# Performance work log

Hardware: AMD Instinct MI355X
Metric: run time of the kernel (lower is better)

## Reference

```python
import jax, jax.numpy as jnp
import numpy as np

N, E = 100000, 600000
IN, H = 164, 128
NH = 4  # attention heads over embed_dim H//4 = 32


def layer_norm(x, g, b, eps=1e-5):
    m = x.mean(-1, keepdims=True)
    v = x.var(-1, keepdims=True)
    return (x - m) * jax.lax.rsqrt(v + eps) * g + b


def gcn_conv(x, W, b, src, dst, n):
    # PyG GCNConv: add self-loops, symmetric D^{-1/2}(A+I)D^{-1/2} normalization.
    deg = jnp.ones((n,), x.dtype).at[dst].add(1.0)  # degree of A+I on target nodes
    dinv = jax.lax.rsqrt(deg)
    xw = x @ W  # [n, out]
    msg = xw[src] * (dinv[src] * dinv[dst])[:, None]  # gather + edge-norm
    agg = jax.ops.segment_sum(msg, dst, num_segments=n)  # scatter-add
    agg = agg + xw * (dinv * dinv)[:, None]  # self-loop term
    return agg + b


def mha_seq1(x, Wq, bq, Wk, bk, Wv, bv, Wo, bo):
    # nn.MultiheadAttention with seq_len==1: softmax over a single key -> weights==1.
    dh = x.shape[-1] // NH
    q = (x @ Wq + bq).reshape(-1, NH, dh)
    k = (x @ Wk + bk).reshape(-1, NH, dh)
    v = (x @ Wv + bv).reshape(-1, NH, dh)
    scores = jnp.sum(q * k, -1, keepdims=True) / jnp.sqrt(jnp.float32(dh))  # [n,NH,1]
    attn = jax.nn.softmax(scores[..., None], axis=-1)[..., 0]  # all ones, kept for fidelity
    out = (attn * v).reshape(-1, NH * dh)
    return out @ Wo + bo


def setup_inputs() -> dict:
    key = jax.random.key(0)
    ks = jax.random.split(key, 16)

    def kaiming(k, i, o):
        return jax.random.normal(k, (i, o), jnp.float32) * (2.0 / i) ** 0.5

    Ha, Hb, Hc = H, H // 2, H // 4  # 128, 64, 32
    return {
        "x": jax.random.normal(ks[0], (N, IN), jnp.float32),
        "edge_index": jax.random.randint(ks[1], (2, E), 0, N),
        "Wi": kaiming(ks[2], IN, Ha), "bi": jnp.zeros((Ha,), jnp.float32),
        "g1": jnp.ones((Ha,), jnp.float32), "b1": jnp.zeros((Ha,), jnp.float32),
        "Wg1": kaiming(ks[3], Ha, Ha), "bg1": jnp.zeros((Ha,), jnp.float32),
        "Wg2": kaiming(ks[4], Ha, Hb), "bg2": jnp.zeros((Hb,), jnp.float32),
        "g2": jnp.ones((Hb,), jnp.float32), "b2": jnp.zeros((Hb,), jnp.float32),
        "Wg3": kaiming(ks[5], Hb, Hc), "bg3": jnp.zeros((Hc,), jnp.float32),
        "Wq": kaiming(ks[6], Hc, Hc), "bq": jnp.zeros((Hc,), jnp.float32),
        "Wk": kaiming(ks[7], Hc, Hc), "bk": jnp.zeros((Hc,), jnp.float32),
        "Wv": kaiming(ks[8], Hc, Hc), "bv": jnp.zeros((Hc,), jnp.float32),
        "Wo": kaiming(ks[9], Hc, Hc), "bo": jnp.zeros((Hc,), jnp.float32),
        "Wc1": kaiming(ks[10], Hc, H // 8), "bc1": jnp.zeros((H // 8,), jnp.float32),
        "Wc2": kaiming(ks[11], H // 8, 32), "bc2": jnp.zeros((32,), jnp.float32),
        "Wc3": kaiming(ks[12], 32, 1), "bc3": jnp.zeros((1,), jnp.float32),
    }


def reference(x, edge_index, Wi, bi, g1, b1, Wg1, bg1, Wg2, bg2, g2, b2,
              Wg3, bg3, Wq, bq, Wk, bk, Wv, bv, Wo, bo,
              Wc1, bc1, Wc2, bc2, Wc3, bc3):
    src, dst = edge_index[0], edge_index[1]
    n = x.shape[0]
    # dropout layers are identity in eval mode
    h = layer_norm(jax.nn.relu(x @ Wi + bi), g1, b1)
    h1 = jax.nn.relu(gcn_conv(h, Wg1, bg1, src, dst, n)) + h
    h2 = layer_norm(jax.nn.relu(gcn_conv(h1, Wg2, bg2, src, dst, n)), g2, b2)
    h3 = jax.nn.relu(gcn_conv(h2, Wg3, bg3, src, dst, n))
    h3 = mha_seq1(h3, Wq, bq, Wk, bk, Wv, bv, Wo, bo)
    h3 = jax.nn.relu(h3 @ Wc1 + bc1)
    h3 = jax.nn.relu(h3 @ Wc2 + bc2)
    return (h3 @ Wc3 + bc3)[:, 0]
```

## Files before the change

kernel.cpp:

```cpp
#include <hip/hip_runtime.h>


typedef __attribute__((ext_vector_type(8))) _Float16 f16x8;
typedef __attribute__((ext_vector_type(4))) _Float16 f16x4;
typedef __attribute__((ext_vector_type(4))) float f32x4;

__global__ void k_count(const int* __restrict__ dst, int* __restrict__ counts, int e) {
  int i = blockIdx.x * blockDim.x + threadIdx.x;
  if (i < e) atomicAdd(&counts[dst[i]], 1);
}

__global__ __launch_bounds__(256) void k_scan_part(
    const int* __restrict__ counts, int* __restrict__ bsums, int n) {
  int tid = threadIdx.x;
  int i0 = blockIdx.x * 1024 + tid * 4;
  int s = 0;
#pragma unroll
  for (int k = 0; k < 4; k++) { int i = i0 + k; if (i < n) s += counts[i]; }
#pragma unroll
  for (int d = 1; d < 64; d <<= 1) s += __shfl_xor(s, d);
  __shared__ int wsum[4];
  int lane = tid & 63, w = tid >> 6;
  if (lane == 0) wsum[w] = s;
  __syncthreads();
  if (tid == 0) bsums[blockIdx.x] = wsum[0] + wsum[1] + wsum[2] + wsum[3];
}

__global__ __launch_bounds__(128) void k_scan_top(int* __restrict__ bsums, int nb) {
  int tid = threadIdx.x;
  int orig = (tid < nb) ? bsums[tid] : 0;
  int v = orig;
  int lane = tid & 63, w = tid >> 6;
#pragma unroll
  for (int d = 1; d < 64; d <<= 1) { int t = __shfl_up(v, d); if (lane >= d) v += t; }
  __shared__ int ws[2];
  if (lane == 63) ws[w] = v;
  __syncthreads();
  if (w == 1) v += ws[0];
  if (tid < nb) bsums[tid] = v - orig;
}

__global__ __launch_bounds__(256) void k_scan_down(
    int* __restrict__ counts, const int* __restrict__ bsums,
    int* __restrict__ offsets, float* __restrict__ dinv, int n, int e) {
  int tid = threadIdx.x;
  int i0 = blockIdx.x * 1024 + tid * 4;
  int c[4]; int tsum = 0;
#pragma unroll
  for (int k = 0; k < 4; k++) { int i = i0 + k; c[k] = (i < n) ? counts[i] : 0; tsum += c[k]; }
  int v = tsum;
  int lane = tid & 63, w = tid >> 6;
#pragma unroll
  for (int d = 1; d < 64; d <<= 1) { int t = __shfl_up(v, d); if (lane >= d) v += t; }
  __shared__ int wsum[4];
  if (lane == 63) wsum[w] = v;
  __syncthreads();
  int wadd = 0;
#pragma unroll
  for (int q = 0; q < 4; q++) if (q < w) wadd += wsum[q];
  int run = (v - tsum) + wadd + bsums[blockIdx.x];
#pragma unroll
  for (int k = 0; k < 4; k++) {
    int i = i0 + k;
    if (i < n) {
      offsets[i] = run;
      dinv[i] = rsqrtf((float)(c[k] + 1));
      counts[i] = 0;
    }
    run += c[k];
  }
  if (blockIdx.x == 0 && tid == 0) offsets[n] = e;
}

__global__ void k_fill(const int* __restrict__ src, const int* __restrict__ dst,
                       const int* __restrict__ offsets, int* __restrict__ cursor,
                       const float* __restrict__ dinv, int2* __restrict__ csr, int e) {
  int i = blockIdx.x * blockDim.x + threadIdx.x;
  if (i >= e) return;
  int s = src[i], d = dst[i];
  int pos = atomicAdd(&cursor[d], 1);
  csr[offsets[d] + pos] = make_int2(s, __float_as_int(dinv[s] * dinv[d]));
}

__device__ __forceinline__ void pack_hi(const float* __restrict__ W,
                                        _Float16* __restrict__ dst,
                                        int K, int N, int u) {
  int lane = u & 63; int rest = u >> 6; int CT = N >> 4;
  int ct = rest % CT, ks = rest / CT;
  int gcol = ct * 16 + (lane & 15);
  int gk0 = ks * 32 + (lane >> 4) * 8;
  size_t o = (size_t)(ks * CT + ct) * 512 + lane * 8;
#pragma unroll
  for (int i = 0; i < 8; i++) {
    float v = (gk0 + i < K) ? W[(size_t)(gk0 + i) * N + gcol] : 0.0f;
    dst[o + i] = (_Float16)v;
  }
}

__device__ __forceinline__ void pack_hl(const float* __restrict__ W,
                                        _Float16* __restrict__ dst,
                                        int K, int N, int u) {
  int lane = u & 63; int rest = u >> 6; int CT = N >> 4;
  int ct = rest % CT, ks = rest / CT;
  int gcol = ct * 16 + (lane & 15);
  int gk0 = ks * 32 + (lane >> 4) * 8;
  size_t oh = (size_t)((ks * CT + ct) * 2) * 512 + lane * 8;
#pragma unroll
  for (int i = 0; i < 8; i++) {
    float v = (gk0 + i < K) ? W[(size_t)(gk0 + i) * N + gcol] : 0.0f;
    _Float16 h = (_Float16)v;
    dst[oh + i] = h;
    dst[oh + 512 + i] = (_Float16)(v - (float)h);
  }
}

__global__ void k_setup(const float* __restrict__ Wi, const float* __restrict__ Wg1,
                        const float* __restrict__ Wg2, const float* __restrict__ Wg3,
                        _Float16* __restrict__ pWi, _Float16* __restrict__ pWg1,
                        _Float16* __restrict__ pWg2, _Float16* __restrict__ pWg3,
                        int* __restrict__ counts, int n) {
  int b = blockIdx.x;
  if (b < 25) {
    int t = b * 256 + threadIdx.x;
    if (t < 3072) pack_hi(Wi, pWi, 164, 128, t);
    else if (t < 5120) pack_hl(Wg1, pWg1, 128, 128, t - 3072);
    else if (t < 6144) pack_hl(Wg2, pWg2, 128, 64, t - 5120);
    else if (t < 6400) pack_hl(Wg3, pWg3, 64, 32, t - 6144);
  } else {
    int i = (b - 25) * 256 + threadIdx.x;
    if (i < n) counts[i] = 0;
  }
}

__global__ __launch_bounds__(512, 4) void k_gemm_in(
    const float* __restrict__ x, const _Float16* __restrict__ pB,
    const float* __restrict__ bias, const float* __restrict__ gamma,
    const float* __restrict__ beta, _Float16* __restrict__ out, int n) {
  constexpr int K = 164, N = 128, CT = 8;
  __shared__ __align__(16) _Float16 sB[6 * CT * 512];
  int tid = threadIdx.x;
  {
    const f16x8* s = (const f16x8*)pB;
    f16x8* d = (f16x8*)sB;
    for (int i = tid; i < 6 * CT * 64; i += 512) d[i] = s[i];
  }
  __syncthreads();
  int lane = tid & 63, w = tid >> 6;
  int row = blockIdx.x * 128 + w * 16 + (lane & 15);
  bool rv = row < n;
  int kof = (lane >> 4) * 8;
  float4 xv[11];
#pragma unroll
  for (int i = 0; i < 11; i++) xv[i] = make_float4(0.f, 0.f, 0.f, 0.f);
  if (rv) {
    const float4* p = (const float4*)(x + (size_t)row * K + kof);
#pragma unroll
    for (int ks = 0; ks < 5; ks++) { xv[2 * ks] = p[ks * 8]; xv[2 * ks + 1] = p[ks * 8 + 1]; }
    if (kof == 0) xv[10] = *(const float4*)(x + (size_t)row * K + 160);
  }
  f32x4 acc[CT];
#pragma unroll
  for (int c = 0; c < CT; c++) acc[c] = (f32x4)0.0f;
#pragma unroll
  for (int ks = 0; ks < 6; ks++) {
    float v[8];
    if (ks < 5) {
      float4 u0 = xv[2 * ks], u1 = xv[2 * ks + 1];
      v[0] = u0.x; v[1] = u0.y; v[2] = u0.z; v[3] = u0.w;
      v[4] = u1.x; v[5] = u1.y; v[6] = u1.z; v[7] = u1.w;
    } else {
      float4 u0 = xv[10];
      v[0] = u0.x; v[1] = u0.y; v[2] = u0.z; v[3] = u0.w;
      v[4] = 0.f; v[5] = 0.f; v[6] = 0.f; v[7] = 0.f;
    }
    f16x8 ah, al;
#pragma unroll
    for (int i = 0; i < 8; i++) {
      ah[i] = (_Float16)v[i];
      al[i] = (_Float16)(v[i] - (float)ah[i]);
    }
#pragma unroll
    for (int c = 0; c < CT; c++) {
      f16x8 b = ((const f16x8*)sB)[(ks * CT + c) * 64 + lane];
      acc[c] = __builtin_amdgcn_mfma_f32_16x16x32_f16(ah, b, acc[c], 0, 0, 0);
      acc[c] = __builtin_amdgcn_mfma_f32_16x16x32_f16(al, b, acc[c], 0, 0, 0);
    }
  }
  int r0 = (lane >> 4) * 4;
  int li = lane & 15;
  float s1[4] = {0, 0, 0, 0}, s2[4] = {0, 0, 0, 0};
#pragma unroll
  for (int c = 0; c < CT; c++) {
    float bb = bias[c * 16 + li];
#pragma unroll
    for (int r = 0; r < 4; r++) {
      float t = acc[c][r] + bb;
      t = t > 0.0f ? t : 0.0f;
      acc[c][r] = t;
      s1[r] += t;
      s2[r] += t * t;
    }
  }
#pragma unroll
  for (int m = 1; m < 16; m <<= 1) {
#pragma unroll
    for (int r = 0; r < 4; r++) {
      s1[r] += __shfl_xor(s1[r], m);
      s2[r] += __shfl_xor(s2[r], m);
    }
  }
#pragma unroll
  for (int c = 0; c < CT; c++) {
    float gv = gamma[c * 16 + li], bv = beta[c * 16 + li];
#pragma unroll
    for (int r = 0; r < 4; r++) {
      int node = blockIdx.x * 128 + w * 16 + r0 + r;
      if (node < n) {
        float mean = s1[r] * (1.0f / N);
        float var = s2[r] * (1.0f / N) - mean * mean;
        float rs = rsqrtf(var + 1e-5f);
        out[(size_t)node * N + c * 16 + li] =
            (_Float16)((acc[c][r] - mean) * rs * gv + bv);
      }
    }
  }
}

template <int K, int N>
__global__ __launch_bounds__(512, 4) void k_gemm_f16(
    const _Float16* __restrict__ A, const _Float16* __restrict__ pB,
    _Float16* __restrict__ out, int n) {
  constexpr int KS = K / 32, CT = N / 16;
  __shared__ __align__(16) _Float16 sB[KS * CT * 1024];
  int tid = threadIdx.x;
  {
    const f16x8* s = (const f16x8*)pB;
    f16x8* d = (f16x8*)sB;
    for (int i = tid; i < KS * CT * 128; i += 512) d[i] = s[i];
  }
  __syncthreads();
  int lane = tid & 63, w = tid >> 6;
  int row = blockIdx.x * 128 + w * 16 + (lane & 15);
  bool rv = row < n;
  const _Float16* ar = A + (size_t)row * K + (lane >> 4) * 8;
  f16x8 av[KS];
#pragma unroll
  for (int ks = 0; ks < KS; ks++) {
    if (rv) av[ks] = *(const f16x8*)(ar + ks * 32);
    else {
#pragma unroll
      for (int i = 0; i < 8; i++) av[ks][i] = (_Float16)0.0f;
    }
  }
  f32x4 acc[CT];
#pragma unroll
  for (int c = 0; c < CT; c++) acc[c] = (f32x4)0.0f;
#pragma unroll
  for (int ks = 0; ks < KS; ks++) {
#pragma unroll
    for (int c = 0; c < CT; c++) {
      f16x8 bh = ((const f16x8*)sB)[((ks * CT + c) * 2) * 64 + lane];
      f16x8 bl = ((const f16x8*)sB)[((ks * CT + c) * 2 + 1) * 64 + lane];
      acc[c] = __builtin_amdgcn_mfma_f32_16x16x32_f16(av[ks], bh, acc[c], 0, 0, 0);
      acc[c] = __builtin_amdgcn_mfma_f32_16x16x32_f16(av[ks], bl, acc[c], 0, 0, 0);
    }
  }
  int r0 = (lane >> 4) * 4;
  int li = lane & 15;
#pragma unroll
  for (int c = 0; c < CT; c++) {
#pragma unroll
    for (int r = 0; r < 4; r++) {
      int node = blockIdx.x * 128 + w * 16 + r0 + r;
      if (node < n) out[(size_t)node * N + c * 16 + li] = (_Float16)acc[c][r];
    }
  }
}

template <int OUT_D, int MODE>
__global__ __launch_bounds__(256, 2) void k_gather(
    const int* __restrict__ off, const int2* __restrict__ csr,
    const _Float16* __restrict__ xw, const float* __restrict__ dinv,
    const float* __restrict__ bias, const _Float16* __restrict__ auxh,
    const float* __restrict__ gamma, const float* __restrict__ beta,
    _Float16* __restrict__ out, int n) {
  constexpr int TPN = OUT_D / 4;
  constexpr int NPB = 256 / TPN;
  int tid = threadIdx.x;
  int node = blockIdx.x * NPB + tid / TPN;
  int li = tid % TPN;
  if (node >= n) return;
  int start = off[node], end = off[node + 1];
  float di = dinv[node];
  float d2 = di * di;
  const _Float16* xp = xw + 4 * li;
  f16x4 self = *(const f16x4*)(xp + (size_t)node * OUT_D);
  f16x4 hres;
  if constexpr (MODE == 0)
    hres = *(const f16x4*)(auxh + (size_t)node * OUT_D + 4 * li);
  float a0 = (float)self[0] * d2 + bias[4 * li + 0];
  float a1 = (float)self[1] * d2 + bias[4 * li + 1];
  float a2 = (float)self[2] * d2 + bias[4 * li + 2];
  float a3 = (float)self[3] * d2 + bias[4 * li + 3];
  for (int cb = start; cb < end; cb += TPN) {
    int m = end - cb; if (m > TPN) m = TPN;
    int sv = node; float nv = 0.0f;
    if (li < m) { int2 me = csr[cb + li]; sv = me.x; nv = __int_as_float(me.y); }
    for (int j0 = 0; j0 < m; j0 += 8) {
      int s0 = __shfl(sv, j0 + 0, TPN), s1 = __shfl(sv, j0 + 1, TPN);
      int s2 = __shfl(sv, j0 + 2, TPN), s3 = __shfl(sv, j0 + 3, TPN);
      int s4 = __shfl(sv, j0 + 4, TPN), s5 = __shfl(sv, j0 + 5, TPN);
      int s6 = __shfl(sv, j0 + 6, TPN), s7 = __shfl(sv, j0 + 7, TPN);
      float w0 = __shfl(nv, j0 + 0, TPN), w1 = __shfl(nv, j0 + 1, TPN);
      float w2 = __shfl(nv, j0 + 2, TPN), w3 = __shfl(nv, j0 + 3, TPN);
      float w4 = __shfl(nv, j0 + 4, TPN), w5 = __shfl(nv, j0 + 5, TPN);
      float w6 = __shfl(nv, j0 + 6, TPN), w7 = __shfl(nv, j0 + 7, TPN);
      f16x4 v0 = *(const f16x4*)(xp + (size_t)s0 * OUT_D);
      f16x4 v1 = *(const f16x4*)(xp + (size_t)s1 * OUT_D);
      f16x4 v2 = *(const f16x4*)(xp + (size_t)s2 * OUT_D);
      f16x4 v3 = *(const f16x4*)(xp + (size_t)s3 * OUT_D);
      f16x4 v4 = *(const f16x4*)(xp + (size_t)s4 * OUT_D);
      f16x4 v5 = *(const f16x4*)(xp + (size_t)s5 * OUT_D);
      f16x4 v6 = *(const f16x4*)(xp + (size_t)s6 * OUT_D);
      f16x4 v7 = *(const f16x4*)(xp + (size_t)s7 * OUT_D);
      a0 += (float)v0[0] * w0 + (float)v1[0] * w1 + (float)v2[0] * w2 + (float)v3[0] * w3
          + (float)v4[0] * w4 + (float)v5[0] * w5 + (float)v6[0] * w6 + (float)v7[0] * w7;
      a1 += (float)v0[1] * w0 + (float)v1[1] * w1 + (float)v2[1] * w2 + (float)v3[1] * w3
          + (float)v4[1] * w4 + (float)v5[1] * w5 + (float)v6[1] * w6 + (float)v7[1] * w7;
      a2 += (float)v0[2] * w0 + (float)v1[2] * w1 + (float)v2[2] * w2 + (float)v3[2] * w3
          + (float)v4[2] * w4 + (float)v5[2] * w5 + (float)v6[2] * w6 + (float)v7[2] * w7;
      a3 += (float)v0[3] * w0 + (float)v1[3] * w1 + (float)v2[3] * w2 + (float)v3[3] * w3
          + (float)v4[3] * w4 + (float)v5[3] * w5 + (float)v6[3] * w6 + (float)v7[3] * w7;
    }
  }
  _Float16* po = out + (size_t)node * OUT_D + 4 * li;
  if constexpr (MODE == 0) {
    f16x4 o;
    o[0] = (_Float16)((a0 > 0.0f ? a0 : 0.0f) + (float)hres[0]);
    o[1] = (_Float16)((a1 > 0.0f ? a1 : 0.0f) + (float)hres[1]);
    o[2] = (_Float16)((a2 > 0.0f ? a2 : 0.0f) + (float)hres[2]);
    o[3] = (_Float16)((a3 > 0.0f ? a3 : 0.0f) + (float)hres[3]);
    *(f16x4*)po = o;
  } else if constexpr (MODE == 1) {
    float v0 = a0 > 0.0f ? a0 : 0.0f, v1 = a1 > 0.0f ? a1 : 0.0f;
    float v2 = a2 > 0.0f ? a2 : 0.0f, v3 = a3 > 0.0f ? a3 : 0.0f;
    float s1 = v0 + v1 + v2 + v3;
    float s2 = v0 * v0 + v1 * v1 + v2 * v2 + v3 * v3;
#pragma unroll
    for (int d = 1; d < TPN; d <<= 1) {
      s1 += __shfl_xor(s1, d, TPN);
      s2 += __shfl_xor(s2, d, TPN);
    }
    float m_ = s1 * (1.0f / OUT_D);
    float var = s2 * (1.0f / OUT_D) - m_ * m_;
    float rs = rsqrtf(var + 1e-5f);
    f16x4 o;
    o[0] = (_Float16)((v0 - m_) * rs * gamma[4 * li + 0] + beta[4 * li + 0]);
    o[1] = (_Float16)((v1 - m_) * rs * gamma[4 * li + 1] + beta[4 * li + 1]);
    o[2] = (_Float16)((v2 - m_) * rs * gamma[4 * li + 2] + beta[4 * li + 2]);
    o[3] = (_Float16)((v3 - m_) * rs * gamma[4 * li + 3] + beta[4 * li + 3]);
    *(f16x4*)po = o;
  } else {
    f16x4 o;
    o[0] = (_Float16)a0; o[1] = (_Float16)a1;
    o[2] = (_Float16)a2; o[3] = (_Float16)a3;
    *(f16x4*)po = o;
  }
}

__global__ __launch_bounds__(256) void k_tail(
    const _Float16* __restrict__ agg3, const float* __restrict__ Wv,
    const float* __restrict__ bv, const float* __restrict__ Wo,
    const float* __restrict__ bo, const float* __restrict__ Wc1,
    const float* __restrict__ bc1, const float* __restrict__ Wc2,
    const float* __restrict__ bc2, const float* __restrict__ Wc3,
    const float* __restrict__ bc3, float* __restrict__ out, int n) {
  __shared__ float sWv[1024], sWo[1024], sWc1[512], sWc2[512];
  __shared__ float sbv[32], sbo[32], sbc2[32], sWc3[32], sbc1[16], sbc3[1];
  int tid = threadIdx.x;
  for (int i = tid; i < 1024; i += 256) { sWv[i] = Wv[i]; sWo[i] = Wo[i]; }
  for (int i = tid; i < 512; i += 256) { sWc1[i] = Wc1[i]; sWc2[i] = Wc2[i]; }
  if (tid < 32) { sbv[tid] = bv[tid]; sbo[tid] = bo[tid];
                  sbc2[tid] = bc2[tid]; sWc3[tid] = Wc3[tid]; }
  if (tid < 16) sbc1[tid] = bc1[tid];
  if (tid == 0) sbc3[0] = bc3[0];
  __syncthreads();
  int node = blockIdx.x * blockDim.x + tid;
  if (node >= n) return;
  float a[32];
  const f16x8* row8 = (const f16x8*)(agg3 + (size_t)node * 32);
#pragma unroll
  for (int q = 0; q < 4; q++) {
    f16x8 t = row8[q];
#pragma unroll
    for (int i = 0; i < 8; i++) {
      float f = (float)t[i];
      a[8 * q + i] = f > 0.0f ? f : 0.0f;
    }
  }
  float v[32];
#pragma unroll
  for (int j = 0; j < 32; j++) v[j] = sbv[j];
  for (int k = 0; k < 32; k++) {
#pragma unroll
    for (int j = 0; j < 32; j++) v[j] += a[k] * sWv[k * 32 + j];
  }
  float o[32];
#pragma unroll
  for (int j = 0; j < 32; j++) o[j] = sbo[j];
  for (int k = 0; k < 32; k++) {
#pragma unroll
    for (int j = 0; j < 32; j++) o[j] += v[k] * sWo[k * 32 + j];
  }
  float c1[16];
#pragma unroll
  for (int j = 0; j < 16; j++) c1[j] = sbc1[j];
  for (int k = 0; k < 32; k++) {
#pragma unroll
    for (int j = 0; j < 16; j++) c1[j] += o[k] * sWc1[k * 16 + j];
  }
#pragma unroll
  for (int j = 0; j < 16; j++) c1[j] = c1[j] > 0.0f ? c1[j] : 0.0f;
  float c2[32];
#pragma unroll
  for (int j = 0; j < 32; j++) c2[j] = sbc2[j];
  for (int k = 0; k < 16; k++) {
#pragma unroll
    for (int j = 0; j < 32; j++) c2[j] += c1[k] * sWc2[k * 32 + j];
  }
  float r = sbc3[0];
#pragma unroll
  for (int k = 0; k < 32; k++) {
    float c = c2[k] > 0.0f ? c2[k] : 0.0f;
    r += c * sWc3[k];
  }
  out[node] = r;
}

extern "C" void kernel_launch(void* const* d_in, const int* in_sizes, int n_in,
                              void* d_out, int out_size, void* d_ws, size_t ws_size,
                              hipStream_t stream) {
  const float* x   = (const float*)d_in[0];
  const int* ei    = (const int*)d_in[1];
  const float* Wi  = (const float*)d_in[2];
  const float* bi  = (const float*)d_in[3];
  const float* g1  = (const float*)d_in[4];
  const float* b1  = (const float*)d_in[5];
  const float* Wg1 = (const float*)d_in[6];
  const float* bg1 = (const float*)d_in[7];
  const float* Wg2 = (const float*)d_in[8];
  const float* bg2 = (const float*)d_in[9];
  const float* g2  = (const float*)d_in[10];
  const float* b2  = (const float*)d_in[11];
  const float* Wg3 = (const float*)d_in[12];
  const float* bg3 = (const float*)d_in[13];
  const float* Wv  = (const float*)d_in[18];
  const float* bv  = (const float*)d_in[19];
  const float* Wo  = (const float*)d_in[20];
  const float* bo  = (const float*)d_in[21];
  const float* Wc1 = (const float*)d_in[22];
  const float* bc1 = (const float*)d_in[23];
  const float* Wc2 = (const float*)d_in[24];
  const float* bc2 = (const float*)d_in[25];
  const float* Wc3 = (const float*)d_in[26];
  const float* bc3 = (const float*)d_in[27];

  const int n = in_sizes[0] / 164;
  const int e = in_sizes[1] / 2;
  const int* src = ei;
  const int* dst = ei + e;

  char* ws = (char*)d_ws;
  size_t off = 0;
  auto alloc = [&](size_t bytes) {
    char* p = ws + off;
    off += (bytes + 255) & ~(size_t)255;
    return p;
  };
  _Float16* A     = (_Float16*)alloc((size_t)n * 128 * 2);
  _Float16* B     = (_Float16*)alloc((size_t)n * 128 * 2);
  _Float16* C     = (_Float16*)alloc((size_t)n * 128 * 2);
  float* dinv     = (float*)alloc((size_t)n * 4);
  int*   counts   = (int*)alloc((size_t)n * 4);
  int*   offsets  = (int*)alloc((size_t)(n + 1) * 4);
  int*   bsums    = (int*)alloc(128 * 4);
  int2*  csr      = (int2*)alloc((size_t)e * 8);
  _Float16* pWi   = (_Float16*)alloc(6 * 8 * 512 * 2);
  _Float16* pWg1  = (_Float16*)alloc(4 * 8 * 1024 * 2);
  _Float16* pWg2  = (_Float16*)alloc(4 * 4 * 1024 * 2);
  _Float16* pWg3  = (_Float16*)alloc(2 * 2 * 1024 * 2);
  (void)ws_size;

  const int BS = 256;
  const int SB = (n + 1023) / 1024;
  const int GB = (n + 127) / 128;

  k_setup<<<25 + (n + 255) / 256, 256, 0, stream>>>(
      Wi, Wg1, Wg2, Wg3, pWi, pWg1, pWg2, pWg3, counts, n);

  k_count<<<(e + BS - 1) / BS, BS, 0, stream>>>(dst, counts, e);
  k_scan_part<<<SB, 256, 0, stream>>>(counts, bsums, n);
  k_scan_top<<<1, 128, 0, stream>>>(bsums, SB);
  k_scan_down<<<SB, 256, 0, stream>>>(counts, bsums, offsets, dinv, n, e);
  k_fill<<<(e + BS - 1) / BS, BS, 0, stream>>>(src, dst, offsets, counts, dinv,
                                               csr, e);

  k_gemm_in<<<GB, 512, 0, stream>>>(x, pWi, bi, g1, b1, A, n);

  k_gemm_f16<128, 128><<<GB, 512, 0, stream>>>(A, pWg1, B, n);
  k_gather<128, 0><<<(n + 7) / 8, 256, 0, stream>>>(
      offsets, csr, B, dinv, bg1, A, nullptr, nullptr, C, n);

  k_gemm_f16<128, 64><<<GB, 512, 0, stream>>>(C, pWg2, A, n);
  k_gather<64, 1><<<(n + 15) / 16, 256, 0, stream>>>(
      offsets, csr, A, dinv, bg2, nullptr, g2, b2, B, n);

  k_gemm_f16<64, 32><<<GB, 512, 0, stream>>>(B, pWg3, A, n);
  k_gather<32, 2><<<(n + 31) / 32, 256, 0, stream>>>(
      offsets, csr, A, dinv, bg3, nullptr, nullptr, nullptr, C, n);

  k_tail<<<(n + BS - 1) / BS, BS, 0, stream>>>(
      C, Wv, bv, Wo, bo, Wc1, bc1, Wc2, bc2, Wc3, bc3, (float*)d_out, n);
}
```

Measured before the change: 226.0 us.

## Drop LDS staging and hi/lo weight split in GEMMs, read weights from global

The GEMM kernels no longer copy packed weights into shared memory behind a barrier; each wave reads its B fragments straight from global memory through the cache. The GCN weight matrices are packed as a single fp16 copy instead of a high/low pair, which halves the MFMA count in k_gemm_f16. The input GEMM now loads x per k-step instead of preloading every chunk into registers. This removes the LDS fill and its sync and cuts matrix work, but it lowers the precision of the GCN weights and makes weight loads rely on L1/L2 hits.

```diff
diff --git a/kernel.cpp b/kernel.cpp
--- a/kernel.cpp
+++ b/kernel.cpp
@@ -94,23 +94,6 @@
   for (int i = 0; i < 8; i++) {
     float v = (gk0 + i < K) ? W[(size_t)(gk0 + i) * N + gcol] : 0.0f;
     dst[o + i] = (_Float16)v;
-  }
-}
-
-__device__ __forceinline__ void pack_hl(const float* __restrict__ W,
-                                        _Float16* __restrict__ dst,
-                                        int K, int N, int u) {
-  int lane = u & 63; int rest = u >> 6; int CT = N >> 4;
-  int ct = rest % CT, ks = rest / CT;
-  int gcol = ct * 16 + (lane & 15);
-  int gk0 = ks * 32 + (lane >> 4) * 8;
-  size_t oh = (size_t)((ks * CT + ct) * 2) * 512 + lane * 8;
-#pragma unroll
-  for (int i = 0; i < 8; i++) {
-    float v = (gk0 + i < K) ? W[(size_t)(gk0 + i) * N + gcol] : 0.0f;
-    _Float16 h = (_Float16)v;
-    dst[oh + i] = h;
-    dst[oh + 512 + i] = (_Float16)(v - (float)h);
   }
 }
 
@@ -123,9 +106,9 @@
   if (b < 25) {
     int t = b * 256 + threadIdx.x;
     if (t < 3072) pack_hi(Wi, pWi, 164, 128, t);
-    else if (t < 5120) pack_hl(Wg1, pWg1, 128, 128, t - 3072);
-    else if (t < 6144) pack_hl(Wg2, pWg2, 128, 64, t - 5120);
-    else if (t < 6400) pack_hl(Wg3, pWg3, 64, 32, t - 6144);
+    else if (t < 5120) pack_hi(Wg1, pWg1, 128, 128, t - 3072);
+    else if (t < 6144) pack_hi(Wg2, pWg2, 128, 64, t - 5120);
+    else if (t < 6400) pack_hi(Wg3, pWg3, 64, 32, t - 6144);
   } else {
     int i = (b - 25) * 256 + threadIdx.x;
     if (i < n) counts[i] = 0;
@@ -137,41 +120,31 @@
     const float* __restrict__ bias, const float* __restrict__ gamma,
     const float* __restrict__ beta, _Float16* __restrict__ out, int n) {
   constexpr int K = 164, N = 128, CT = 8;
-  __shared__ __align__(16) _Float16 sB[6 * CT * 512];
-  int tid = threadIdx.x;
-  {
-    const f16x8* s = (const f16x8*)pB;
-    f16x8* d = (f16x8*)sB;
-    for (int i = tid; i < 6 * CT * 64; i += 512) d[i] = s[i];
-  }
-  __syncthreads();
+  int tid = threadIdx.x;
   int lane = tid & 63, w = tid >> 6;
   int row = blockIdx.x * 128 + w * 16 + (lane & 15);
   bool rv = row < n;
   int kof = (lane >> 4) * 8;
-  float4 xv[11];
-#pragma unroll
-  for (int i = 0; i < 11; i++) xv[i] = make_float4(0.f, 0.f, 0.f, 0.f);
-  if (rv) {
-    const float4* p = (const float4*)(x + (size_t)row * K + kof);
-#pragma unroll
-    for (int ks = 0; ks < 5; ks++) { xv[2 * ks] = p[ks * 8]; xv[2 * ks + 1] = p[ks * 8 + 1]; }
-    if (kof == 0) xv[10] = *(const float4*)(x + (size_t)row * K + 160);
-  }
+  const f16x8* Bf = (const f16x8*)pB;
   f32x4 acc[CT];
 #pragma unroll
   for (int c = 0; c < CT; c++) acc[c] = (f32x4)0.0f;
 #pragma unroll
   for (int ks = 0; ks < 6; ks++) {
+    int gk = ks * 32 + kof;
     float v[8];
-    if (ks < 5) {
-      float4 u0 = xv[2 * ks], u1 = xv[2 * ks + 1];
+    if (rv && gk + 8 <= K) {
+      const float4* p = (const float4*)(x + (size_t)row * K + gk);
+      float4 u0 = p[0], u1 = p[1];
       v[0] = u0.x; v[1] = u0.y; v[2] = u0.z; v[3] = u0.w;
       v[4] = u1.x; v[5] = u1.y; v[6] = u1.z; v[7] = u1.w;
-    } else {
-      float4 u0 = xv[10];
+    } else if (rv && gk < K) {
+      float4 u0 = *(const float4*)(x + (size_t)row * K + gk);
       v[0] = u0.x; v[1] = u0.y; v[2] = u0.z; v[3] = u0.w;
       v[4] = 0.f; v[5] = 0.f; v[6] = 0.f; v[7] = 0.f;
+    } else {
+#pragma unroll
+      for (int i = 0; i < 8; i++) v[i] = 0.0f;
     }
     f16x8 ah, al;
 #pragma unroll
@@ -181,7 +154,7 @@
     }
 #pragma unroll
     for (int c = 0; c < CT; c++) {
-      f16x8 b = ((const f16x8*)sB)[(ks * CT + c) * 64 + lane];
+      f16x8 b = Bf[(ks * CT + c) * 64 + lane];
       acc[c] = __builtin_amdgcn_mfma_f32_16x16x32_f16(ah, b, acc[c], 0, 0, 0);
       acc[c] = __builtin_amdgcn_mfma_f32_16x16x32_f16(al, b, acc[c], 0, 0, 0);
     }
@@ -231,18 +204,12 @@
     const _Float16* __restrict__ A, const _Float16* __restrict__ pB,
     _Float16* __restrict__ out, int n) {
   constexpr int KS = K / 32, CT = N / 16;
-  __shared__ __align__(16) _Float16 sB[KS * CT * 1024];
-  int tid = threadIdx.x;
-  {
-    const f16x8* s = (const f16x8*)pB;
-    f16x8* d = (f16x8*)sB;
-    for (int i = tid; i < KS * CT * 128; i += 512) d[i] = s[i];
-  }
-  __syncthreads();
+  int tid = threadIdx.x;
   int lane = tid & 63, w = tid >> 6;
   int row = blockIdx.x * 128 + w * 16 + (lane & 15);
   bool rv = row < n;
   const _Float16* ar = A + (size_t)row * K + (lane >> 4) * 8;
+  const f16x8* Bf = (const f16x8*)pB;
   f16x8 av[KS];
 #pragma unroll
   for (int ks = 0; ks < KS; ks++) {
@@ -259,10 +226,8 @@
   for (int ks = 0; ks < KS; ks++) {
 #pragma unroll
     for (int c = 0; c < CT; c++) {
-      f16x8 bh = ((const f16x8*)sB)[((ks * CT + c) * 2) * 64 + lane];
-      f16x8 bl = ((const f16x8*)sB)[((ks * CT + c) * 2 + 1) * 64 + lane];
-      acc[c] = __builtin_amdgcn_mfma_f32_16x16x32_f16(av[ks], bh, acc[c], 0, 0, 0);
-      acc[c] = __builtin_amdgcn_mfma_f32_16x16x32_f16(av[ks], bl, acc[c], 0, 0, 0);
+      f16x8 b = Bf[(ks * CT + c) * 64 + lane];
+      acc[c] = __builtin_amdgcn_mfma_f32_16x16x32_f16(av[ks], b, acc[c], 0, 0, 0);
     }
   }
   int r0 = (lane >> 4) * 4;
@@ -485,10 +450,10 @@
   int*   offsets  = (int*)alloc((size_t)(n + 1) * 4);
   int*   bsums    = (int*)alloc(128 * 4);
   int2*  csr      = (int2*)alloc((size_t)e * 8);
-  _Float16* pWi   = (_Float16*)alloc(6 * 8 * 512 * 2);
-  _Float16* pWg1  = (_Float16*)alloc(4 * 8 * 1024 * 2);
-  _Float16* pWg2  = (_Float16*)alloc(4 * 4 * 1024 * 2);
-  _Float16* pWg3  = (_Float16*)alloc(2 * 2 * 1024 * 2);
+  _Float16* pWi   = (_Float16*)alloc(3072 * 16);
+  _Float16* pWg1  = (_Float16*)alloc(2048 * 16);
+  _Float16* pWg2  = (_Float16*)alloc(1024 * 16);
+  _Float16* pWg3  = (_Float16*)alloc(256 * 16);
   (void)ws_size;
 
   const int BS = 256;
```

Measured after the change: 234.3 us. 1.04x slower.
